# Kernel optimization log

Measured on AMD Instinct MI355X. Metric: run time of the kernel, lower is better.

The kernel has to match this reference:

```python
import jax, jax.numpy as jnp
import numpy as np

EMBED_DIM = 512
NUM_HEADS = 8
K_NEAREST = 5
B = 8192
N_MEM = 50000


def setup_inputs() -> dict:
    key = jax.random.key(0)
    ks = jax.random.split(key, 12)
    E = EMBED_DIM
    s = 1.0 / np.sqrt(E)
    inp = {
        "Q": jax.random.normal(ks[0], (B, E), jnp.float32),
        "mem_keys": jax.random.normal(ks[1], (N_MEM, E), jnp.float32),
        "mem_vals": jax.random.normal(ks[2], (N_MEM, E), jnp.float32),
        # pre-projection linears (linear_q/k/v)
        "Wq": jax.random.uniform(ks[3], (E, E), jnp.float32, -s, s),
        "bq": jnp.zeros((E,), jnp.float32),
        "Wk": jax.random.uniform(ks[4], (E, E), jnp.float32, -s, s),
        "bk": jnp.zeros((E,), jnp.float32),
        "Wv": jax.random.uniform(ks[5], (E, E), jnp.float32, -s, s),
        "bv": jnp.zeros((E,), jnp.float32),
        # nn.MultiheadAttention internal in/out projections
        "W_in_q": jax.random.uniform(ks[6], (E, E), jnp.float32, -s, s),
        "W_in_k": jax.random.uniform(ks[7], (E, E), jnp.float32, -s, s),
        "W_in_v": jax.random.uniform(ks[8], (E, E), jnp.float32, -s, s),
        "b_in": jnp.zeros((3 * E,), jnp.float32),
        "W_out": jax.random.uniform(ks[9], (E, E), jnp.float32, -s, s),
        "b_out": jnp.zeros((E,), jnp.float32),
    }
    return inp


def _find_k_nearest(Q, mem_keys, mem_vals, k):
    # squared Euclidean distance; argmax of negative distance == k nearest
    # dists: [B, N]
    sq = jnp.sum(mem_keys * mem_keys, axis=-1)  # [N]
    scores = 2.0 * (Q @ mem_keys.T) - sq[None, :]  # -||q-m||^2 up to const
    _, idx = jax.lax.top_k(scores, k)  # [B, k]
    K = mem_keys[idx]  # [B, k, E]
    V = mem_vals[idx]  # [B, k, E]
    return K, V


def _mha(Q, K, V, W_in_q, W_in_k, W_in_v, b_in, W_out, b_out):
    # Q: [B,1,E], K/V: [B,k,E]; torch nn.MultiheadAttention, batch_first
    E = Q.shape[-1]
    H = NUM_HEADS
    d = E // H
    q = Q @ W_in_q.T + b_in[:E]
    k = K @ W_in_k.T + b_in[E:2 * E]
    v = V @ W_in_v.T + b_in[2 * E:]
    Bsz = Q.shape[0]
    q = q.reshape(Bsz, -1, H, d).transpose(0, 2, 1, 3)  # [B,H,1,d]
    k = k.reshape(Bsz, -1, H, d).transpose(0, 2, 1, 3)  # [B,H,k,d]
    v = v.reshape(Bsz, -1, H, d).transpose(0, 2, 1, 3)
    scores = jnp.einsum("bhqd,bhkd->bhqk", q, k) / jnp.sqrt(jnp.float32(d))
    attn = jax.nn.softmax(scores, axis=-1)
    out = jnp.einsum("bhqk,bhkd->bhqd", attn, v)
    out = out.transpose(0, 2, 1, 3).reshape(Bsz, -1, E)
    return out @ W_out.T + b_out


def reference(Q, mem_keys, mem_vals, Wq, bq, Wk, bk, Wv, bv,
              W_in_q, W_in_k, W_in_v, b_in, W_out, b_out):
    K, V = _find_k_nearest(Q, mem_keys, mem_vals, K_NEAREST)
    Qs = Q[:, None, :]  # [B,1,E]
    Qp = Qs @ Wq.T + bq
    Kp = K @ Wk.T + bk
    Vp = V @ Wv.T + bv
    return _mha(Qp, Kp, Vp, W_in_q, W_in_k, W_in_v, b_in, W_out, b_out)
```

## Files before the change

kernel.cpp:

```cpp
#include <hip/hip_runtime.h>
#include <hip/hip_bf16.h>
#include <hip/hip_fp16.h>

typedef _Float16 f16;
typedef _Float16 f16x8 __attribute__((ext_vector_type(8)));
typedef float f32x4 __attribute__((ext_vector_type(4)));

constexpr int EE     = 512;
constexpr int NMEM   = 50000;
constexpr int BQ     = 8192;
constexpr int NSEG   = 16;
constexpr int SEGLEN = NMEM / NSEG;
constexpr int KVT    = 32;
constexpr int NT32   = (SEGLEN + KVT - 1) / KVT;
constexpr int NC     = 5;
constexpr int NCAND  = NSEG * NC;
constexpr int NRES   = 10;

typedef const __attribute__((address_space(1))) unsigned char* gas_t;
typedef __attribute__((address_space(3))) unsigned char* las_t;
__device__ static inline void g2l16(const void* g, void* l) {
  __builtin_amdgcn_global_load_lds((gas_t)g, (las_t)l, 16, 0, 0);
}

__global__ __launch_bounds__(256) void k_prep_keys(const float* __restrict__ mk,
                                                   f16* __restrict__ kh,
                                                   float* __restrict__ sq32,
                                                   double* __restrict__ sq64) {
  int row  = blockIdx.x * 4 + (threadIdx.x >> 6);
  int lane = threadIdx.x & 63;
  const float4* src = (const float4*)(mk + (size_t)row * EE) + lane * 2;
  float4 a = src[0], b = src[1];
  double s = (double)a.x*a.x + (double)a.y*a.y + (double)a.z*a.z + (double)a.w*a.w
           + (double)b.x*b.x + (double)b.y*b.y + (double)b.z*b.z + (double)b.w*b.w;
  f16x8 h;
  h[0]=(f16)a.x; h[1]=(f16)a.y; h[2]=(f16)a.z; h[3]=(f16)a.w;
  h[4]=(f16)b.x; h[5]=(f16)b.y; h[6]=(f16)b.z; h[7]=(f16)b.w;
  *((f16x8*)(kh + (size_t)row * EE) + lane) = h;
  #pragma unroll
  for (int o = 32; o > 0; o >>= 1) s += __shfl_down(s, o);
  if (lane == 0) { sq64[row] = s; sq32[row] = (float)s; }
}

__global__ __launch_bounds__(256) void k_prep_f16(const float* __restrict__ src,
                                                  f16* __restrict__ dst) {
  int row  = blockIdx.x * 4 + (threadIdx.x >> 6);
  int lane = threadIdx.x & 63;
  const float4* s = (const float4*)(src + (size_t)row * EE) + lane * 2;
  float4 a = s[0], b = s[1];
  f16x8 h;
  h[0]=(f16)a.x; h[1]=(f16)a.y; h[2]=(f16)a.z; h[3]=(f16)a.w;
  h[4]=(f16)b.x; h[5]=(f16)b.y; h[6]=(f16)b.z; h[7]=(f16)b.w;
  *((f16x8*)(dst + (size_t)row * EE) + lane) = h;
}

__global__ __launch_bounds__(256) void k_compose(const float* __restrict__ Wq, const float* __restrict__ Wk,
                                                 const float* __restrict__ Wv, const float* __restrict__ Wiq,
                                                 const float* __restrict__ Wik, const float* __restrict__ Wiv,
                                                 f16* __restrict__ Wc) {
  int m = blockIdx.z;
  const float* A = (m == 0) ? Wiq : ((m == 1) ? Wik : Wiv);
  const float* B = (m == 0) ? Wq  : ((m == 1) ? Wk  : Wv);
  f16* C = Wc + (size_t)m * EE * EE;
  __shared__ float As[64][33];
  __shared__ float Bs[32][65];
  int i0 = blockIdx.x * 64, j0 = blockIdx.y * 64;
  int tx = threadIdx.x & 15, ty = threadIdx.x >> 4;
  float acc[4][4] = {};
  for (int kb = 0; kb < EE; kb += 32) {
    __syncthreads();
    #pragma unroll
    for (int v = 0; v < 8; ++v) {
      int idx = threadIdx.x + v * 256;
      As[idx >> 5][idx & 31] = A[(size_t)(i0 + (idx >> 5)) * EE + kb + (idx & 31)];
    }
    #pragma unroll
    for (int v = 0; v < 8; ++v) {
      int idx = threadIdx.x + v * 256;
      Bs[idx >> 6][idx & 63] = B[(size_t)(kb + (idx >> 6)) * EE + j0 + (idx & 63)];
    }
    __syncthreads();
    for (int t = 0; t < 32; ++t) {
      float av[4], bv[4];
      #pragma unroll
      for (int u = 0; u < 4; ++u) av[u] = As[ty*4+u][t];
      #pragma unroll
      for (int u = 0; u < 4; ++u) bv[u] = Bs[t][tx*4+u];
      #pragma unroll
      for (int a = 0; a < 4; ++a)
        #pragma unroll
        for (int b = 0; b < 4; ++b) acc[a][b] = fmaf(av[a], bv[b], acc[a][b]);
    }
  }
  #pragma unroll
  for (int a = 0; a < 4; ++a)
    #pragma unroll
    for (int b = 0; b < 4; ++b)
      C[(size_t)(i0 + ty*4 + a) * EE + j0 + tx*4 + b] = (f16)acc[a][b];
}

__global__ void k_bias(const float* __restrict__ Wiq, const float* __restrict__ Wik,
                       const float* __restrict__ Wiv, const float* __restrict__ bqv,
                       const float* __restrict__ bkv, const float* __restrict__ bvv,
                       const float* __restrict__ b_in, float* __restrict__ bc) {
  int m = blockIdx.x;
  const float* Wi = (m == 0) ? Wiq : ((m == 1) ? Wik : Wiv);
  const float* bb = (m == 0) ? bqv : ((m == 1) ? bkv : bvv);
  for (int i = threadIdx.x; i < EE; i += blockDim.x) {
    float s = 0.f;
    for (int t = 0; t < EE; ++t) s = fmaf(Wi[(size_t)i * EE + t], bb[t], s);
    bc[m * EE + i] = s + b_in[m * EE + i];
  }
}

__global__ void k_cvtw(const float* __restrict__ W, f16* __restrict__ Wo) {
  int i = blockIdx.x * 256 + threadIdx.x;
  Wo[i] = (f16)W[i];
}

__global__ __launch_bounds__(256, 2) void k_stage1(const f16* __restrict__ Qh,
                                                   const f16* __restrict__ Kh,
                                                   const float* __restrict__ sq32,
                                                   int* __restrict__ part_i,
                                                   float* __restrict__ part_s) {
  const int rb  = blockIdx.x;
  const int seg = blockIdx.y;
  const int tid = threadIdx.x;
  const int w   = tid >> 6;
  const int l   = tid & 63;
  const int lc  = l & 15, lp = l >> 4;
  const int seg_start = seg * SEGLEN;
  const int seg_end   = seg_start + SEGLEN;

  __shared__ f16   Bt[2][KVT * 520];
  __shared__ float sqs[2][KVT];

  const int rowbase = rb * 128 + w * 32;
  f16x8 a0[16], a1[16];
  {
    const f16* base0 = Qh + (size_t)(rowbase + lc) * EE + lp * 8;
    const f16* base1 = base0 + (size_t)16 * EE;
    #pragma unroll
    for (int ks = 0; ks < 16; ++ks) {
      asm volatile("global_load_dwordx4 %0, %1, off"
                   : "=v"(a0[ks]) : "v"(base0 + ks * 32) : "memory");
      asm volatile("global_load_dwordx4 %0, %1, off"
                   : "=v"(a1[ks]) : "v"(base1 + ks * 32) : "memory");
    }
    asm volatile("s_waitcnt vmcnt(0)" ::: "memory");
    __builtin_amdgcn_sched_barrier(0);
  }

  float ts0[NC], ts1[NC]; int ti0[NC], ti1[NC];
  #pragma unroll
  for (int i = 0; i < NC; ++i) {
    ts0[i] = -3.0e38f; ti0[i] = 0;
    ts1[i] = -3.0e38f; ti1[i] = 0;
  }

#define INS(TS, TI, SV, IV) do { \
    if ((SV) > TS[NC-1]) { \
      TS[NC-1] = (SV); TI[NC-1] = (IV); \
      _Pragma("unroll") \
      for (int _i = NC - 1; _i > 0; --_i) { \
        if (TS[_i] > TS[_i-1]) { \
          float _tf = TS[_i]; TS[_i] = TS[_i-1]; TS[_i-1] = _tf; \
          int   _tx = TI[_i]; TI[_i] = TI[_i-1]; TI[_i-1] = _tx; \
        } \
      } \
    } \
  } while (0)

  #define STAGE(buf, tt) do { \
      int kk = seg_start + (tt) * KVT; \
      _Pragma("unroll") \
      for (int j = 0; j < 8; ++j) { \
        int key = kk + w * 8 + j; \
        key = key < NMEM ? key : NMEM - 1; \
        g2l16(Kh + (size_t)key * EE + l * 8, &Bt[buf][(w*8 + j) * 520]); \
      } \
      if (tid < KVT) { \
        int kq = kk + tid; \
        float v = 6.0e38f; \
        if (kq < seg_end) v = sq32[kq]; \
        sqs[buf][tid] = v; \
      } \
    } while (0)

  STAGE(0, 0);
  for (int t = 0; t < NT32; ++t) {
    const int c = t & 1;
    __syncthreads();
    if (t + 1 < NT32) STAGE(c ^ 1, t + 1);

    f32x4 A00 = {0,0,0,0}, A01 = {0,0,0,0}, A10 = {0,0,0,0}, A11 = {0,0,0,0};
    #pragma unroll
    for (int ks = 0; ks < 16; ++ks) {
      f16x8 kf0 = *(const f16x8*)&Bt[c][lc * 520 + ks * 32 + lp * 8];
      f16x8 kf1 = *(const f16x8*)&Bt[c][(16 + lc) * 520 + ks * 32 + lp * 8];
      A00 = __builtin_amdgcn_mfma_f32_16x16x32_f16(kf0, a0[ks], A00, 0, 0, 0);
      A01 = __builtin_amdgcn_mfma_f32_16x16x32_f16(kf0, a1[ks], A01, 0, 0, 0);
      A10 = __builtin_amdgcn_mfma_f32_16x16x32_f16(kf1, a0[ks], A10, 0, 0, 0);
      A11 = __builtin_amdgcn_mfma_f32_16x16x32_f16(kf1, a1[ks], A11, 0, 0, 0);
    }
    f32x4 q0 = *(const f32x4*)&sqs[c][lp * 4];
    f32x4 q1 = *(const f32x4*)&sqs[c][16 + lp * 4];
    f32x4 s00 = 2.0f * A00 - q0;
    f32x4 s01 = 2.0f * A01 - q0;
    f32x4 s10 = 2.0f * A10 - q1;
    f32x4 s11 = 2.0f * A11 - q1;
    const int kb = seg_start + t * KVT;
    const int b0 = kb + lp * 4;
    const int b1 = b0 + 16;
    #pragma unroll
    for (int r = 0; r < 4; ++r) {
      INS(ts0, ti0, s00[r], b0 + r);
      INS(ts0, ti0, s10[r], b1 + r);
      INS(ts1, ti1, s01[r], b0 + r);
      INS(ts1, ti1, s11[r], b1 + r);
    }
  }
  #undef STAGE

  #pragma unroll
  for (int d = 16; d <= 32; d <<= 1) {
    float os[NC]; int oi[NC];
    #pragma unroll
    for (int i = 0; i < NC; ++i) { os[i] = __shfl_xor(ts0[i], d); oi[i] = __shfl_xor(ti0[i], d); }
    #pragma unroll
    for (int j = 0; j < NC; ++j) INS(ts0, ti0, os[j], oi[j]);
    #pragma unroll
    for (int i = 0; i < NC; ++i) { os[i] = __shfl_xor(ts1[i], d); oi[i] = __shfl_xor(ti1[i], d); }
    #pragma unroll
    for (int j = 0; j < NC; ++j) INS(ts1, ti1, os[j], oi[j]);
  }
#undef INS
  if (l < 16) {
    int row = rowbase + lc;
    #pragma unroll
    for (int i = 0; i < NC; ++i) {
      part_i[(size_t)row * NCAND + seg * NC + i] = ti0[i];
      part_s[(size_t)row * NCAND + seg * NC + i] = ts0[i];
    }
  } else if (l < 32) {
    int row = rowbase + 16 + lc;
    #pragma unroll
    for (int i = 0; i < NC; ++i) {
      part_i[(size_t)row * NCAND + seg * NC + i] = ti1[i];
      part_s[(size_t)row * NCAND + seg * NC + i] = ts1[i];
    }
  }
}

__global__ __launch_bounds__(64) void k_rescore(const float* __restrict__ Q,
                                                const float* __restrict__ mk,
                                                const double* __restrict__ sq64,
                                                const int* __restrict__ part_i,
                                                const float* __restrict__ part_s,
                                                int* __restrict__ idx5) {
  const int row = blockIdx.x;
  const int l = threadIdx.x;
  const float* Qr = Q + (size_t)row * EE;
  float q[8];
  #pragma unroll
  for (int i = 0; i < 8; ++i) q[i] = Qr[l + 64*i];
  float s0 = part_s[(size_t)row * NCAND + l];
  int   i0 = part_i[(size_t)row * NCAND + l];
  float s1 = (l < NCAND - 64) ? part_s[(size_t)row * NCAND + 64 + l] : -3.0e38f;
  int   i1 = (l < NCAND - 64) ? part_i[(size_t)row * NCAND + 64 + l] : 0;

  double bs[5] = {-1e300, -1e300, -1e300, -1e300, -1e300};
  int    bi[5] = {0, 0, 0, 0, 0};
  #pragma unroll
  for (int p = 0; p < NRES; ++p) {
    bool pick0 = (s0 >= s1);
    float m  = pick0 ? s0 : s1;
    int   mi = pick0 ? i0 : i1;
    int   code = (l << 1) | (pick0 ? 0 : 1);
    #pragma unroll
    for (int o = 32; o > 0; o >>= 1) {
      float mo = __shfl_xor(m, o);
      int   io = __shfl_xor(mi, o);
      int   co = __shfl_xor(code, o);
      if (mo > m || (mo == m && co < code)) { m = mo; mi = io; code = co; }
    }
    if ((code >> 1) == l) { if (code & 1) s1 = -3.0e38f; else s0 = -3.0e38f; }
    const float* kr = mk + (size_t)mi * EE;
    double pd = 0.0;
    #pragma unroll
    for (int i = 0; i < 8; ++i) pd += (double)q[i] * (double)kr[l + 64*i];
    #pragma unroll
    for (int o = 32; o > 0; o >>= 1) pd += __shfl_down(pd, o);
    if (l == 0) {
      double s = 2.0 * pd - sq64[mi];
      if (s > bs[4]) {
        bs[4] = s; bi[4] = mi;
        #pragma unroll
        for (int i = 4; i > 0; --i) {
          if (bs[i] > bs[i-1]) {
            double tf = bs[i]; bs[i] = bs[i-1]; bs[i-1] = tf;
            int    tx = bi[i]; bi[i] = bi[i-1]; bi[i-1] = tx;
          }
        }
      }
    }
  }
  if (l == 0) {
    #pragma unroll
    for (int i = 0; i < 5; ++i) idx5[(size_t)row*5 + i] = bi[i];
  }
}

template <int OUTF32>
__global__ __launch_bounds__(256) void k_gemm(const f16* __restrict__ A, const f16* __restrict__ B,
                                              const float* __restrict__ bias, void* __restrict__ outp) {
  __shared__ f16 As[64][72];
  __shared__ f16 Bs[64][72];
  const int tid = threadIdx.x;
  const int wv = tid >> 6, l = tid & 63, lc = l & 15, lp = l >> 4;
  const int m0 = blockIdx.x * 64, n0 = blockIdx.y * 64;
  const int r = tid >> 2, co = (tid & 3) * 16;
  f32x4 acc[4] = {{0,0,0,0},{0,0,0,0},{0,0,0,0},{0,0,0,0}};
  for (int kb = 0; kb < EE; kb += 64) {
    __syncthreads();
    *(float4*)&As[r][co]     = *(const float4*)(A + (size_t)(m0 + r) * EE + kb + co);
    *(float4*)&As[r][co + 8] = *(const float4*)(A + (size_t)(m0 + r) * EE + kb + co + 8);
    *(float4*)&Bs[r][co]     = *(const float4*)(B + (size_t)(n0 + r) * EE + kb + co);
    *(float4*)&Bs[r][co + 8] = *(const float4*)(B + (size_t)(n0 + r) * EE + kb + co + 8);
    __syncthreads();
    #pragma unroll
    for (int ks = 0; ks < 2; ++ks) {
      f16x8 a = *(const f16x8*)&As[wv*16 + lc][ks*32 + lp*8];
      #pragma unroll
      for (int f = 0; f < 4; ++f) {
        f16x8 b = *(const f16x8*)&Bs[f*16 + lc][ks*32 + lp*8];
        acc[f] = __builtin_amdgcn_mfma_f32_16x16x32_f16(a, b, acc[f], 0, 0, 0);
      }
    }
  }
  #pragma unroll
  for (int f = 0; f < 4; ++f) {
    int col = n0 + f*16 + lc;
    float bsv = bias[col];
    #pragma unroll
    for (int rr = 0; rr < 4; ++rr) {
      int row = m0 + wv*16 + lp*4 + rr;
      float v = acc[f][rr] + bsv;
      if (OUTF32) ((float*)outp)[(size_t)row * EE + col] = v;
      else        ((f16*)outp)[(size_t)row * EE + col] = (f16)v;
    }
  }
}

template <int AF16>
__global__ __launch_bounds__(256) void k_gemm_g(const int* __restrict__ gidx, const void* __restrict__ Asrc,
                                                const f16* __restrict__ B, const float* __restrict__ bias,
                                                f16* __restrict__ outp) {
  __shared__ f16 As[64][72];
  __shared__ f16 Bs[64][72];
  const int tid = threadIdx.x;
  const int wv = tid >> 6, l = tid & 63, lc = l & 15, lp = l >> 4;
  const int m0 = blockIdx.x * 64, n0 = blockIdx.y * 64;
  const int r = tid >> 2, co = (tid & 3) * 16;
  const int gi = gidx[m0 + r];
  f32x4 acc[4] = {{0,0,0,0},{0,0,0,0},{0,0,0,0},{0,0,0,0}};
  for (int kb = 0; kb < EE; kb += 64) {
    __syncthreads();
    if (AF16) {
      const f16* arow = (const f16*)Asrc + (size_t)gi * EE;
      *(f16x8*)&As[r][co]     = *(const f16x8*)(arow + kb + co);
      *(f16x8*)&As[r][co + 8] = *(const f16x8*)(arow + kb + co + 8);
    } else {
      const float* arow = (const float*)Asrc + (size_t)gi * EE;
      float4 x0 = *(const float4*)(arow + kb + co);
      float4 x1 = *(const float4*)(arow + kb + co + 4);
      float4 x2 = *(const float4*)(arow + kb + co + 8);
      float4 x3 = *(const float4*)(arow + kb + co + 12);
      f16x8 h0, h1;
      h0[0]=(f16)x0.x; h0[1]=(f16)x0.y; h0[2]=(f16)x0.z; h0[3]=(f16)x0.w;
      h0[4]=(f16)x1.x; h0[5]=(f16)x1.y; h0[6]=(f16)x1.z; h0[7]=(f16)x1.w;
      h1[0]=(f16)x2.x; h1[1]=(f16)x2.y; h1[2]=(f16)x2.z; h1[3]=(f16)x2.w;
      h1[4]=(f16)x3.x; h1[5]=(f16)x3.y; h1[6]=(f16)x3.z; h1[7]=(f16)x3.w;
      *(f16x8*)&As[r][co]     = h0;
      *(f16x8*)&As[r][co + 8] = h1;
    }
    *(float4*)&Bs[r][co]     = *(const float4*)(B + (size_t)(n0 + r) * EE + kb + co);
    *(float4*)&Bs[r][co + 8] = *(const float4*)(B + (size_t)(n0 + r) * EE + kb + co + 8);
    __syncthreads();
    #pragma unroll
    for (int ks = 0; ks < 2; ++ks) {
      f16x8 a = *(const f16x8*)&As[wv*16 + lc][ks*32 + lp*8];
      #pragma unroll
      for (int f = 0; f < 4; ++f) {
        f16x8 b = *(const f16x8*)&Bs[f*16 + lc][ks*32 + lp*8];
        acc[f] = __builtin_amdgcn_mfma_f32_16x16x32_f16(a, b, acc[f], 0, 0, 0);
      }
    }
  }
  #pragma unroll
  for (int f = 0; f < 4; ++f) {
    int col = n0 + f*16 + lc;
    float bsv = bias[col];
    #pragma unroll
    for (int rr = 0; rr < 4; ++rr) {
      int row = m0 + wv*16 + lp*4 + rr;
      outp[(size_t)row * EE + col] = (f16)(acc[f][rr] + bsv);
    }
  }
}

__global__ __launch_bounds__(256) void k_attn(const f16* __restrict__ qp, const f16* __restrict__ kp,
                                              const f16* __restrict__ vp, f16* __restrict__ ao) {
  int row = blockIdx.x * 4 + (threadIdx.x >> 6);
  int l = threadIdx.x & 63;
  int h = l >> 3, sl = l & 7;
  const f16* q = qp + (size_t)row * EE + h * 64 + sl * 8;
  float qv[8];
  #pragma unroll
  for (int i = 0; i < 8; ++i) qv[i] = (float)q[i];
  float sc[5];
  #pragma unroll
  for (int j = 0; j < 5; ++j) {
    const f16* kr = kp + ((size_t)row * 5 + j) * EE + h * 64 + sl * 8;
    float p = 0.f;
    #pragma unroll
    for (int i = 0; i < 8; ++i) p = fmaf(qv[i], (float)kr[i], p);
    p += __shfl_xor(p, 1); p += __shfl_xor(p, 2); p += __shfl_xor(p, 4);
    sc[j] = p * 0.125f;
  }
  float mx = fmaxf(fmaxf(fmaxf(sc[0], sc[1]), fmaxf(sc[2], sc[3])), sc[4]);
  float sum = 0.f;
  #pragma unroll
  for (int j = 0; j < 5; ++j) { sc[j] = __expf(sc[j] - mx); sum += sc[j]; }
  float inv = 1.0f / sum;
  float o[8] = {};
  #pragma unroll
  for (int j = 0; j < 5; ++j) {
    const f16* vr = vp + ((size_t)row * 5 + j) * EE + h * 64 + sl * 8;
    float aw = sc[j] * inv;
    #pragma unroll
    for (int i = 0; i < 8; ++i) o[i] = fmaf(aw, (float)vr[i], o[i]);
  }
  f16* dst = ao + (size_t)row * EE + h * 64 + sl * 8;
  #pragma unroll
  for (int i = 0; i < 8; ++i) dst[i] = (f16)o[i];
}

extern "C" void kernel_launch(void* const* d_in, const int* in_sizes, int n_in,
                              void* d_out, int out_size, void* d_ws, size_t ws_size,
                              hipStream_t stream) {
  const float* Q    = (const float*)d_in[0];
  const float* mk   = (const float*)d_in[1];
  const float* mv   = (const float*)d_in[2];
  const float* Wq   = (const float*)d_in[3];
  const float* bq   = (const float*)d_in[4];
  const float* Wk   = (const float*)d_in[5];
  const float* bk   = (const float*)d_in[6];
  const float* Wv   = (const float*)d_in[7];
  const float* bv   = (const float*)d_in[8];
  const float* Wiq  = (const float*)d_in[9];
  const float* Wik  = (const float*)d_in[10];
  const float* Wiv  = (const float*)d_in[11];
  const float* b_in = (const float*)d_in[12];
  const float* Wo   = (const float*)d_in[13];
  const float* bo   = (const float*)d_in[14];

  char* w = (char*)d_ws;
  size_t off = 0;
  auto alloc = [&](size_t bytes) { size_t o = off; off += (bytes + 255) & ~(size_t)255; return (void*)(w + o); };
  f16*    Kh     = (f16*)   alloc((size_t)NMEM * EE * 2);
  f16*    Qh     = (f16*)   alloc((size_t)BQ * EE * 2);
  float*  sq32   = (float*) alloc((size_t)NMEM * 4);
  double* sq64   = (double*)alloc((size_t)NMEM * 8);
  f16*    Wc     = (f16*)   alloc((size_t)3 * EE * EE * 2);
  f16*    Wo16   = (f16*)   alloc((size_t)EE * EE * 2);
  float*  bc     = (float*) alloc((size_t)3 * EE * 4);
  int*    part_i = (int*)   alloc((size_t)BQ * NCAND * 4);
  float*  part_s = (float*) alloc((size_t)BQ * NCAND * 4);
  int*    idx5   = (int*)   alloc((size_t)BQ * 5 * 4);
  f16*    qp     = (f16*)   alloc((size_t)BQ * EE * 2);
  f16*    vp     = (f16*)   alloc((size_t)BQ * 5 * EE * 2);
  f16*    ao     = Qh;
  size_t need_big = off + (size_t)NMEM * EE * 2 + (size_t)BQ * 5 * EE * 2 + 4096;
  bool big = (ws_size >= need_big);
  f16* Vh = nullptr;
  f16* kp;
  if (big) {
    Vh = (f16*)alloc((size_t)NMEM * EE * 2);
    kp = (f16*)alloc((size_t)BQ * 5 * EE * 2);
  } else {
    kp = Kh;
  }
  (void)in_sizes; (void)n_in; (void)out_size;

  k_prep_keys<<<NMEM / 4, 256, 0, stream>>>(mk, Kh, sq32, sq64);
  k_prep_f16<<<BQ / 4, 256, 0, stream>>>(Q, Qh);
  if (big) k_prep_f16<<<NMEM / 4, 256, 0, stream>>>(mv, Vh);
  k_compose<<<dim3(8, 8, 3), 256, 0, stream>>>(Wq, Wk, Wv, Wiq, Wik, Wiv, Wc);
  k_bias<<<3, 256, 0, stream>>>(Wiq, Wik, Wiv, bq, bk, bv, b_in, bc);
  k_cvtw<<<(EE * EE) / 256, 256, 0, stream>>>(Wo, Wo16);
  k_stage1<<<dim3(BQ / 128, NSEG), 256, 0, stream>>>(Qh, Kh, sq32, part_i, part_s);
  k_rescore<<<BQ, 64, 0, stream>>>(Q, mk, sq64, part_i, part_s, idx5);
  k_gemm<0><<<dim3(BQ / 64, 8), 256, 0, stream>>>(Qh, Wc, bc, qp);
  if (big) {
    k_gemm_g<1><<<dim3(BQ * 5 / 64, 8), 256, 0, stream>>>(idx5, Kh, Wc + (size_t)EE * EE, bc + EE, kp);
    k_gemm_g<1><<<dim3(BQ * 5 / 64, 8), 256, 0, stream>>>(idx5, Vh, Wc + (size_t)2 * EE * EE, bc + 2 * EE, vp);
  } else {
    k_gemm_g<0><<<dim3(BQ * 5 / 64, 8), 256, 0, stream>>>(idx5, mk, Wc + (size_t)EE * EE, bc + EE, kp);
    k_gemm_g<0><<<dim3(BQ * 5 / 64, 8), 256, 0, stream>>>(idx5, mv, Wc + (size_t)2 * EE * EE, bc + 2 * EE, vp);
  }
  k_attn<<<BQ / 4, 256, 0, stream>>>(qp, kp, vp, ao);
  k_gemm<1><<<dim3(BQ / 64, 8), 256, 0, stream>>>(ao, Wo16, bo, (float*)d_out);
}
```

Baseline: 792.9 us.

## Pack candidate index into score mantissa and widen projection GEMM tiles

```diff
diff --git a/kernel.cpp b/kernel.cpp
--- a/kernel.cpp
+++ b/kernel.cpp
@@ -21,6 +21,10 @@
 typedef __attribute__((address_space(3))) unsigned char* las_t;
 __device__ static inline void g2l16(const void* g, void* l) {
   __builtin_amdgcn_global_load_lds((gas_t)g, (las_t)l, 16, 0, 0);
+}
+
+__device__ static inline float pack_si(float s, int li) {
+  return __uint_as_float((__float_as_uint(s) & 0xFFFFF000u) | (unsigned)li);
 }
 
 __global__ __launch_bounds__(256) void k_prep_keys(const float* __restrict__ mk,
@@ -151,22 +155,19 @@
     __builtin_amdgcn_sched_barrier(0);
   }
 
-  float ts0[NC], ts1[NC]; int ti0[NC], ti1[NC];
-  #pragma unroll
-  for (int i = 0; i < NC; ++i) {
-    ts0[i] = -3.0e38f; ti0[i] = 0;
-    ts1[i] = -3.0e38f; ti1[i] = 0;
-  }
-
-#define INS(TS, TI, SV, IV) do { \
-    if ((SV) > TS[NC-1]) { \
-      TS[NC-1] = (SV); TI[NC-1] = (IV); \
+  float ts0[NC], ts1[NC];
+  #pragma unroll
+  for (int i = 0; i < NC; ++i) { ts0[i] = -3.0e38f; ts1[i] = -3.0e38f; }
+
+#define INS1(TS, PV) do { \
+    if (__ballot((PV) > TS[NC-1])) { \
+      float _nv = ((PV) > TS[NC-1]) ? (PV) : TS[NC-1]; \
+      TS[NC-1] = _nv; \
       _Pragma("unroll") \
       for (int _i = NC - 1; _i > 0; --_i) { \
-        if (TS[_i] > TS[_i-1]) { \
-          float _tf = TS[_i]; TS[_i] = TS[_i-1]; TS[_i-1] = _tf; \
-          int   _tx = TI[_i]; TI[_i] = TI[_i-1]; TI[_i-1] = _tx; \
-        } \
+        float _mx = fmaxf(TS[_i], TS[_i-1]); \
+        float _mn = fminf(TS[_i], TS[_i-1]); \
+        TS[_i-1] = _mx; TS[_i] = _mn; \
       } \
     } \
   } while (0)
@@ -209,44 +210,45 @@
     f32x4 s01 = 2.0f * A01 - q0;
     f32x4 s10 = 2.0f * A10 - q1;
     f32x4 s11 = 2.0f * A11 - q1;
-    const int kb = seg_start + t * KVT;
-    const int b0 = kb + lp * 4;
-    const int b1 = b0 + 16;
+    const int li0 = t * KVT + lp * 4;
+    const int li1 = li0 + 16;
     #pragma unroll
     for (int r = 0; r < 4; ++r) {
-      INS(ts0, ti0, s00[r], b0 + r);
-      INS(ts0, ti0, s10[r], b1 + r);
-      INS(ts1, ti1, s01[r], b0 + r);
-      INS(ts1, ti1, s11[r], b1 + r);
+      INS1(ts0, pack_si(s00[r], li0 + r));
+      INS1(ts0, pack_si(s10[r], li1 + r));
+      INS1(ts1, pack_si(s01[r], li0 + r));
+      INS1(ts1, pack_si(s11[r], li1 + r));
     }
   }
   #undef STAGE
 
   #pragma unroll
   for (int d = 16; d <= 32; d <<= 1) {
-    float os[NC]; int oi[NC];
-    #pragma unroll
-    for (int i = 0; i < NC; ++i) { os[i] = __shfl_xor(ts0[i], d); oi[i] = __shfl_xor(ti0[i], d); }
-    #pragma unroll
-    for (int j = 0; j < NC; ++j) INS(ts0, ti0, os[j], oi[j]);
-    #pragma unroll
-    for (int i = 0; i < NC; ++i) { os[i] = __shfl_xor(ts1[i], d); oi[i] = __shfl_xor(ti1[i], d); }
-    #pragma unroll
-    for (int j = 0; j < NC; ++j) INS(ts1, ti1, os[j], oi[j]);
-  }
-#undef INS
+    float os[NC];
+    #pragma unroll
+    for (int i = 0; i < NC; ++i) os[i] = __shfl_xor(ts0[i], d);
+    #pragma unroll
+    for (int j = 0; j < NC; ++j) INS1(ts0, os[j]);
+    #pragma unroll
+    for (int i = 0; i < NC; ++i) os[i] = __shfl_xor(ts1[i], d);
+    #pragma unroll
+    for (int j = 0; j < NC; ++j) INS1(ts1, os[j]);
+  }
+#undef INS1
   if (l < 16) {
     int row = rowbase + lc;
     #pragma unroll
     for (int i = 0; i < NC; ++i) {
-      part_i[(size_t)row * NCAND + seg * NC + i] = ti0[i];
+      unsigned u = __float_as_uint(ts0[i]);
+      part_i[(size_t)row * NCAND + seg * NC + i] = seg_start + (int)(u & 0xFFFu);
       part_s[(size_t)row * NCAND + seg * NC + i] = ts0[i];
     }
   } else if (l < 32) {
     int row = rowbase + 16 + lc;
     #pragma unroll
     for (int i = 0; i < NC; ++i) {
-      part_i[(size_t)row * NCAND + seg * NC + i] = ti1[i];
+      unsigned u = __float_as_uint(ts1[i]);
+      part_i[(size_t)row * NCAND + seg * NC + i] = seg_start + (int)(u & 0xFFFu);
       part_s[(size_t)row * NCAND + seg * NC + i] = ts1[i];
     }
   }
@@ -311,100 +313,73 @@
   }
 }
 
-template <int OUTF32>
-__global__ __launch_bounds__(256) void k_gemm(const f16* __restrict__ A, const f16* __restrict__ B,
-                                              const float* __restrict__ bias, void* __restrict__ outp) {
-  __shared__ f16 As[64][72];
+template <int GATHER, int AF16, int OUTF32>
+__global__ __launch_bounds__(256) void k_pgemm128(const int* __restrict__ gidx, const void* __restrict__ Asrc,
+                                                  const f16* __restrict__ B, const float* __restrict__ bias,
+                                                  void* __restrict__ outp) {
+  __shared__ f16 As[128][72];
   __shared__ f16 Bs[64][72];
   const int tid = threadIdx.x;
   const int wv = tid >> 6, l = tid & 63, lc = l & 15, lp = l >> 4;
-  const int m0 = blockIdx.x * 64, n0 = blockIdx.y * 64;
-  const int r = tid >> 2, co = (tid & 3) * 16;
-  f32x4 acc[4] = {{0,0,0,0},{0,0,0,0},{0,0,0,0},{0,0,0,0}};
+  const int m0 = blockIdx.x * 128, n0 = blockIdx.y * 64;
+  const int r0 = tid >> 3;
+  const int cb = (tid & 7) * 8;
+  const f16*   arf[4];
+  const float* ar32[4];
+  #pragma unroll
+  for (int v = 0; v < 4; ++v) {
+    int row = m0 + r0 + v * 32;
+    int gi = GATHER ? gidx[row] : row;
+    if (AF16) arf[v]  = (const f16*)Asrc + (size_t)gi * EE;
+    else      ar32[v] = (const float*)Asrc + (size_t)gi * EE;
+  }
+  const f16* br0 = B + (size_t)(n0 + r0) * EE;
+  const f16* br1 = B + (size_t)(n0 + r0 + 32) * EE;
+  f32x4 acc[2][4] = {{{0,0,0,0},{0,0,0,0},{0,0,0,0},{0,0,0,0}},
+                     {{0,0,0,0},{0,0,0,0},{0,0,0,0},{0,0,0,0}}};
   for (int kb = 0; kb < EE; kb += 64) {
     __syncthreads();
-    *(float4*)&As[r][co]     = *(const float4*)(A + (size_t)(m0 + r) * EE + kb + co);
-    *(float4*)&As[r][co + 8] = *(const float4*)(A + (size_t)(m0 + r) * EE + kb + co + 8);
-    *(float4*)&Bs[r][co]     = *(const float4*)(B + (size_t)(n0 + r) * EE + kb + co);
-    *(float4*)&Bs[r][co + 8] = *(const float4*)(B + (size_t)(n0 + r) * EE + kb + co + 8);
+    #pragma unroll
+    for (int v = 0; v < 4; ++v) {
+      if (AF16) {
+        *(f16x8*)&As[r0 + v*32][cb] = *(const f16x8*)(arf[v] + kb + cb);
+      } else {
+        float4 x0 = *(const float4*)(ar32[v] + kb + cb);
+        float4 x1 = *(const float4*)(ar32[v] + kb + cb + 4);
+        f16x8 h;
+        h[0]=(f16)x0.x; h[1]=(f16)x0.y; h[2]=(f16)x0.z; h[3]=(f16)x0.w;
+        h[4]=(f16)x1.x; h[5]=(f16)x1.y; h[6]=(f16)x1.z; h[7]=(f16)x1.w;
+        *(f16x8*)&As[r0 + v*32][cb] = h;
+      }
+    }
+    *(f16x8*)&Bs[r0][cb]      = *(const f16x8*)(br0 + kb + cb);
+    *(f16x8*)&Bs[r0 + 32][cb] = *(const f16x8*)(br1 + kb + cb);
     __syncthreads();
     #pragma unroll
     for (int ks = 0; ks < 2; ++ks) {
-      f16x8 a = *(const f16x8*)&As[wv*16 + lc][ks*32 + lp*8];
+      f16x8 a0 = *(const f16x8*)&As[wv*32 + lc][ks*32 + lp*8];
+      f16x8 a1 = *(const f16x8*)&As[wv*32 + 16 + lc][ks*32 + lp*8];
       #pragma unroll
       for (int f = 0; f < 4; ++f) {
         f16x8 b = *(const f16x8*)&Bs[f*16 + lc][ks*32 + lp*8];
-        acc[f] = __builtin_amdgcn_mfma_f32_16x16x32_f16(a, b, acc[f], 0, 0, 0);
+        acc[0][f] = __builtin_amdgcn_mfma_f32_16x16x32_f16(a0, b, acc[0][f], 0, 0, 0);
+        acc[1][f] = __builtin_amdgcn_mfma_f32_16x16x32_f16(a1, b, acc[1][f], 0, 0, 0);
       }
     }
   }
   #pragma unroll
-  for (int f = 0; f < 4; ++f) {
-    int col = n0 + f*16 + lc;
-    float bsv = bias[col];
-    #pragma unroll
-    for (int rr = 0; rr < 4; ++rr) {
-      int row = m0 + wv*16 + lp*4 + rr;
-      float v = acc[f][rr] + bsv;
-      if (OUTF32) ((float*)outp)[(size_t)row * EE + col] = v;
-      else        ((f16*)outp)[(size_t)row * EE + col] = (f16)v;
-    }
-  }
-}
-
-template <int AF16>
-__global__ __launch_bounds__(256) void k_gemm_g(const int* __restrict__ gidx, const void* __restrict__ Asrc,
-                                                const f16* __restrict__ B, const float* __restrict__ bias,
-                                                f16* __restrict__ outp) {
-  __shared__ f16 As[64][72];
-  __shared__ f16 Bs[64][72];
-  const int tid = threadIdx.x;
-  const int wv = tid >> 6, l = tid & 63, lc = l & 15, lp = l >> 4;
-  const int m0 = blockIdx.x * 64, n0 = blockIdx.y * 64;
-  const int r = tid >> 2, co = (tid & 3) * 16;
-  const int gi = gidx[m0 + r];
-  f32x4 acc[4] = {{0,0,0,0},{0,0,0,0},{0,0,0,0},{0,0,0,0}};
-  for (int kb = 0; kb < EE; kb += 64) {
-    __syncthreads();
-    if (AF16) {
-      const f16* arow = (const f16*)Asrc + (size_t)gi * EE;
-      *(f16x8*)&As[r][co]     = *(const f16x8*)(arow + kb + co);
-      *(f16x8*)&As[r][co + 8] = *(const f16x8*)(arow + kb + co + 8);
-    } else {
-      const float* arow = (const float*)Asrc + (size_t)gi * EE;
-      float4 x0 = *(const float4*)(arow + kb + co);
-      float4 x1 = *(const float4*)(arow + kb + co + 4);
-      float4 x2 = *(const float4*)(arow + kb + co + 8);
-      float4 x3 = *(const float4*)(arow + kb + co + 12);
-      f16x8 h0, h1;
-      h0[0]=(f16)x0.x; h0[1]=(f16)x0.y; h0[2]=(f16)x0.z; h0[3]=(f16)x0.w;
-      h0[4]=(f16)x1.x; h0[5]=(f16)x1.y; h0[6]=(f16)x1.z; h0[7]=(f16)x1.w;
-      h1[0]=(f16)x2.x; h1[1]=(f16)x2.y; h1[2]=(f16)x2.z; h1[3]=(f16)x2.w;
-      h1[4]=(f16)x3.x; h1[5]=(f16)x3.y; h1[6]=(f16)x3.z; h1[7]=(f16)x3.w;
-      *(f16x8*)&As[r][co]     = h0;
-      *(f16x8*)&As[r][co + 8] = h1;
-    }
-    *(float4*)&Bs[r][co]     = *(const float4*)(B + (size_t)(n0 + r) * EE + kb + co);
-    *(float4*)&Bs[r][co + 8] = *(const float4*)(B + (size_t)(n0 + r) * EE + kb + co + 8);
-    __syncthreads();
-    #pragma unroll
-    for (int ks = 0; ks < 2; ++ks) {
-      f16x8 a = *(const f16x8*)&As[wv*16 + lc][ks*32 + lp*8];
+  for (int g = 0; g < 2; ++g) {
+    #pragma unroll
+    for (int f = 0; f < 4; ++f) {
+      int col = n0 + f*16 + lc;
+      float bsv = bias[col];
       #pragma unroll
-      for (int f = 0; f < 4; ++f) {
-        f16x8 b = *(const f16x8*)&Bs[f*16 + lc][ks*32 + lp*8];
-        acc[f] = __builtin_amdgcn_mfma_f32_16x16x32_f16(a, b, acc[f], 0, 0, 0);
+      for (int rr = 0; rr < 4; ++rr) {
+        int row = m0 + wv*32 + g*16 + lp*4 + rr;
+        float v = acc[g][f][rr] + bsv;
+        if (OUTF32) ((float*)outp)[(size_t)row * EE + col] = v;
+        else        ((f16*)outp)[(size_t)row * EE + col] = (f16)v;
       }
-    }
-  }
-  #pragma unroll
-  for (int f = 0; f < 4; ++f) {
-    int col = n0 + f*16 + lc;
-    float bsv = bias[col];
-    #pragma unroll
-    for (int rr = 0; rr < 4; ++rr) {
-      int row = m0 + wv*16 + lp*4 + rr;
-      outp[(size_t)row * EE + col] = (f16)(acc[f][rr] + bsv);
     }
   }
 }
@@ -501,14 +476,14 @@
   k_cvtw<<<(EE * EE) / 256, 256, 0, stream>>>(Wo, Wo16);
   k_stage1<<<dim3(BQ / 128, NSEG), 256, 0, stream>>>(Qh, Kh, sq32, part_i, part_s);
   k_rescore<<<BQ, 64, 0, stream>>>(Q, mk, sq64, part_i, part_s, idx5);
-  k_gemm<0><<<dim3(BQ / 64, 8), 256, 0, stream>>>(Qh, Wc, bc, qp);
+  k_pgemm128<0,1,0><<<dim3(BQ / 128, 8), 256, 0, stream>>>(nullptr, Qh, Wc, bc, qp);
   if (big) {
-    k_gemm_g<1><<<dim3(BQ * 5 / 64, 8), 256, 0, stream>>>(idx5, Kh, Wc + (size_t)EE * EE, bc + EE, kp);
-    k_gemm_g<1><<<dim3(BQ * 5 / 64, 8), 256, 0, stream>>>(idx5, Vh, Wc + (size_t)2 * EE * EE, bc + 2 * EE, vp);
+    k_pgemm128<1,1,0><<<dim3(BQ * 5 / 128, 8), 256, 0, stream>>>(idx5, Kh, Wc + (size_t)EE * EE, bc + EE, kp);
+    k_pgemm128<1,1,0><<<dim3(BQ * 5 / 128, 8), 256, 0, stream>>>(idx5, Vh, Wc + (size_t)2 * EE * EE, bc + 2 * EE, vp);
   } else {
-    k_gemm_g<0><<<dim3(BQ * 5 / 64, 8), 256, 0, stream>>>(idx5, mk, Wc + (size_t)EE * EE, bc + EE, kp);
-    k_gemm_g<0><<<dim3(BQ * 5 / 64, 8), 256, 0, stream>>>(idx5, mv, Wc + (size_t)2 * EE * EE, bc + 2 * EE, vp);
+    k_pgemm128<1,0,0><<<dim3(BQ * 5 / 128, 8), 256, 0, stream>>>(idx5, mk, Wc + (size_t)EE * EE, bc + EE, kp);
+    k_pgemm128<1,0,0><<<dim3(BQ * 5 / 128, 8), 256, 0, stream>>>(idx5, mv, Wc + (size_t)2 * EE * EE, bc + 2 * EE, vp);
   }
   k_attn<<<BQ / 4, 256, 0, stream>>>(qp, kp, vp, ao);
-  k_gemm<1><<<dim3(BQ / 64, 8), 256, 0, stream>>>(ao, Wo16, bo, (float*)d_out);
-}
+  k_pgemm128<0,1,1><<<dim3(BQ / 128, 8), 256, 0, stream>>>(nullptr, ao, Wo16, bo, d_out);
+}
```

Result: faster. 746.6 us (-5.8%).
